# Kernel optimization log

Hardware: AMD Instinct MI355X
Metric: run time of the kernel (lower is better)

## Reference

```python
import jax, jax.numpy as jnp
import numpy as np

B, N, DIN, DMID, DOUT, E = 64, 5000, 64, 128, 32, 80000


def setup_inputs() -> dict:
    key = jax.random.key(0)
    ks = jax.random.split(key, 12)
    p = lambda k, shape: jax.random.normal(k, shape, jnp.float32) * 0.05
    return {
        "x": jax.random.normal(ks[0], (B, N, DIN), jnp.float32),
        "edge_index": jax.random.randint(ks[1], (2, E), 0, N),
        "prev_hidden_state": jax.random.normal(ks[2], (B, N, DMID), jnp.float32),
        # GCNConv weights/biases for gates z, r, h
        "Wg_z": p(ks[3], (DIN, DMID)), "bg_z": jnp.zeros((DMID,), jnp.float32),
        "Wg_r": p(ks[4], (DIN, DMID)), "bg_r": jnp.zeros((DMID,), jnp.float32),
        "Wg_h": p(ks[5], (DIN, DMID)), "bg_h": jnp.zeros((DMID,), jnp.float32),
        # gate Linear layers on concat([conv_out, H]) -> DMID
        "Wl_z": p(ks[6], (2 * DMID, DMID)), "bl_z": jnp.zeros((DMID,), jnp.float32),
        "Wl_r": p(ks[7], (2 * DMID, DMID)), "bl_r": jnp.zeros((DMID,), jnp.float32),
        "Wl_h": p(ks[8], (2 * DMID, DMID)), "bl_h": jnp.zeros((DMID,), jnp.float32),
        # final output Linear
        "W_out": p(ks[9], (DMID, DOUT)), "b_out": jnp.zeros((DOUT,), jnp.float32),
    }


def reference(x, edge_index, prev_hidden_state,
              Wg_z, bg_z, Wg_r, bg_r, Wg_h, bg_h,
              Wl_z, bl_z, Wl_r, bl_r, Wl_h, bl_h,
              W_out, b_out):
    # GCN symmetric normalization with self-loops (pyg gcn_norm, improved=False)
    row, col = edge_index[0], edge_index[1]
    loop = jnp.arange(N)
    src = jnp.concatenate([row, loop])          # [E+N]
    dst = jnp.concatenate([col, loop])          # [E+N]
    ew = jnp.ones((E + N,), x.dtype)
    deg = jnp.zeros((N,), x.dtype).at[dst].add(ew)
    dis = jnp.where(deg > 0, jax.lax.rsqrt(jnp.maximum(deg, 1e-12)), 0.0)
    norm = dis[src] * ew * dis[dst]             # [E+N]

    def gcn(w, b):
        xw = jnp.einsum('bnd,de->bne', x, w)            # [B,N,DMID]
        msg = xw[:, src, :] * norm[None, :, None]       # gather + weight
        out = jnp.zeros((B, N, w.shape[1]), x.dtype).at[:, dst, :].add(msg)
        return out + b

    H = prev_hidden_state
    Z = jax.nn.sigmoid(jnp.concatenate([gcn(Wg_z, bg_z), H], -1) @ Wl_z + bl_z)
    R = jax.nn.sigmoid(jnp.concatenate([gcn(Wg_r, bg_r), H], -1) @ Wl_r + bl_r)
    Ht = jnp.tanh(jnp.concatenate([gcn(Wg_h, bg_h), H * R], -1) @ Wl_h + bl_h)
    H_new = Z * H + (1.0 - Z) * Ht                      # [B,N,DMID]

    y = jnp.mean(H_new, axis=1)                         # MeanAggregation over nodes
    y = jax.nn.relu(y) @ W_out + b_out                  # [B,DOUT]
    return (y, H_new)
```

## Files before the change

### kernel.cpp

```cpp
#include <hip/hip_runtime.h>
#include <cmath>

namespace {

constexpr int B = 64, N = 5000, DIN = 64, DMID = 128, DOUT = 32, E = 80000;
constexpr int NT = (N + 63) / 64;

typedef unsigned short u16;
typedef __attribute__((ext_vector_type(8))) short short8;
typedef __attribute__((ext_vector_type(4))) float floatx4;

#define MFMA16(a, b, c) __builtin_amdgcn_mfma_f32_16x16x32_bf16((a), (b), (c), 0, 0, 0)

__device__ __forceinline__ u16 f2bf(float f) {
  union { float f; unsigned u; } v; v.f = f;
  unsigned r = v.u + 0x7FFFu + ((v.u >> 16) & 1u);
  return (u16)(r >> 16);
}
__device__ __forceinline__ float bf2f(u16 s) {
  union { unsigned u; float f; } v; v.u = ((unsigned)s) << 16;
  return v.f;
}
__device__ __forceinline__ float sigmoid_fast(float x) {
  return __builtin_amdgcn_rcpf(1.f + __expf(-x));
}
__device__ __forceinline__ float tanh_fast(float x) {
  return fmaf(2.f, __builtin_amdgcn_rcpf(1.f + __expf(-2.f * x)), -1.f);
}


__global__ void count_kernel(const int* __restrict__ ei, int* counts) {
  int e = blockIdx.x * 256 + threadIdx.x;
  if (e < E) atomicAdd(&counts[ei[E + e]], 1);
}

__global__ void scan_kernel(int* counts, int* rowptr, float* dis) {
  __shared__ int sdata[1024];
  const int tid = threadIdx.x;
  constexpr int CH = (N + 1023) / 1024;
  int local[CH], cnt[CH];
  int s = 0;
  for (int i = 0; i < CH; i++) {
    int idx = tid * CH + i;
    int c = (idx < N) ? counts[idx] : 0;
    cnt[i] = c;
    local[i] = s;
    s += c;
  }
  sdata[tid] = s;
  __syncthreads();
  for (int off = 1; off < 1024; off <<= 1) {
    int v = (tid >= off) ? sdata[tid - off] : 0;
    __syncthreads();
    sdata[tid] += v;
    __syncthreads();
  }
  int prev = (tid > 0) ? sdata[tid - 1] : 0;
  for (int i = 0; i < CH; i++) {
    int idx = tid * CH + i;
    if (idx < N) {
      rowptr[idx] = prev + local[i];
      dis[idx] = rsqrtf((float)(cnt[i] + 1));
      counts[idx] = 0;
    }
  }
  if (tid == 1023) rowptr[N] = sdata[1023];
}

__global__ void fill_kernel(const int* __restrict__ ei, const int* __restrict__ rowptr,
                            const float* __restrict__ dis, int* counts,
                            int* csr_src, float* csr_w) {
  int e = blockIdx.x * 256 + threadIdx.x;
  if (e >= E) return;
  int r = ei[e], c = ei[E + e];
  int pos = rowptr[c] + atomicAdd(&counts[c], 1);
  csr_src[pos] = r;
  csr_w[pos] = dis[r] * dis[c];
}


__global__ void pack_kernel(const float* Wgz, const float* Wgr, const float* Wgh,
                            const float* Wlz, const float* Wlr, const float* Wlh,
                            const float* bgz, const float* bgr, const float* bgh,
                            const float* blz, const float* blr, const float* blh,
                            u16* wcB, u16* whB, float* bcAll) {
  int t = blockIdx.x * 256 + threadIdx.x;
  const float* Wg[3] = {Wgz, Wgr, Wgh};
  const float* Wl[3] = {Wlz, Wlr, Wlh};
  const float* bg[3] = {bgz, bgr, bgh};
  const float* bl[3] = {blz, blr, blh};
  if (t < 48 * 64) {
    int chunk = t >> 6, lane = t & 63;
    int q = lane >> 4, lm = lane & 15;
    int g = chunk >> 4, rem = chunk & 15, kt = rem >> 3, nt = rem & 7;
    int n = nt * 16 + lm;
#pragma unroll
    for (int jj = 0; jj < 8; jj++) {
      int k = kt * 32 + q * 8 + jj;
      float acc = 0.f;
      for (int j = 0; j < DMID; j++)
        acc = fmaf(Wg[g][k * DMID + j], Wl[g][j * DMID + n], acc);
      wcB[(size_t)(chunk * 64 + lane) * 8 + jj] = f2bf(acc);
    }
  } else if (t < 48 * 64 + 96 * 64) {
    int t2 = t - 48 * 64;
    int chunk = t2 >> 6, lane = t2 & 63;
    int q = lane >> 4, lm = lane & 15;
    int g = chunk >> 5, rem = chunk & 31, kt = rem >> 3, nt = rem & 7;
    int n = nt * 16 + lm;
#pragma unroll
    for (int jj = 0; jj < 8; jj++) {
      int k = kt * 32 + q * 8 + jj;
      whB[(size_t)t2 * 8 + jj] = f2bf(Wl[g][(DMID + k) * DMID + n]);
    }
  } else {
    int t3 = t - 48 * 64 - 96 * 64;
    if (t3 < 384) {
      int g = t3 >> 7, n = t3 & 127;
      float acc = bl[g][n];
      for (int j = 0; j < DMID; j++)
        acc = fmaf(bg[g][j], Wl[g][j * DMID + n], acc);
      bcAll[t3] = acc;
    }
  }
}


__global__ __launch_bounds__(256) void agg_kernel(
    const float* __restrict__ x, const int* __restrict__ rowptr,
    const int* __restrict__ csr_src, const float* __restrict__ csr_w,
    const float* __restrict__ dis, u16* __restrict__ xs) {
  constexpr int G = B * N / 16;
  const int bid = blockIdx.x;
  const int nb = (bid & 7) * (G >> 3) + (bid >> 3);
  const int sub = threadIdx.x >> 4;
  const int l16 = threadIdx.x & 15;
  const int unit = nb * 16 + sub;
  const int b = unit / N;
  const int n = unit - b * N;
  const float* xb = x + (size_t)b * N * DIN;
  const float d = dis[n];
  float4 v = *(const float4*)(xb + (size_t)n * DIN + l16 * 4);
  const float sw = d * d;
  float ax = v.x * sw, ay = v.y * sw, az = v.z * sw, aw = v.w * sw;
  const int s1 = rowptr[n + 1];
  int p = rowptr[n];
  for (; p + 4 <= s1; p += 4) {
    int i0 = csr_src[p], i1 = csr_src[p + 1], i2 = csr_src[p + 2], i3 = csr_src[p + 3];
    float w0 = csr_w[p], w1 = csr_w[p + 1], w2 = csr_w[p + 2], w3 = csr_w[p + 3];
    float4 a0 = *(const float4*)(xb + (size_t)i0 * DIN + l16 * 4);
    float4 a1 = *(const float4*)(xb + (size_t)i1 * DIN + l16 * 4);
    float4 a2 = *(const float4*)(xb + (size_t)i2 * DIN + l16 * 4);
    float4 a3 = *(const float4*)(xb + (size_t)i3 * DIN + l16 * 4);
    ax = fmaf(a0.x, w0, ax); ay = fmaf(a0.y, w0, ay);
    az = fmaf(a0.z, w0, az); aw = fmaf(a0.w, w0, aw);
    ax = fmaf(a1.x, w1, ax); ay = fmaf(a1.y, w1, ay);
    az = fmaf(a1.z, w1, az); aw = fmaf(a1.w, w1, aw);
    ax = fmaf(a2.x, w2, ax); ay = fmaf(a2.y, w2, ay);
    az = fmaf(a2.z, w2, az); aw = fmaf(a2.w, w2, aw);
    ax = fmaf(a3.x, w3, ax); ay = fmaf(a3.y, w3, ay);
    az = fmaf(a3.z, w3, az); aw = fmaf(a3.w, w3, aw);
  }
  for (; p < s1; p++) {
    int i0 = csr_src[p];
    float w0 = csr_w[p];
    float4 a0 = *(const float4*)(xb + (size_t)i0 * DIN + l16 * 4);
    ax = fmaf(a0.x, w0, ax); ay = fmaf(a0.y, w0, ay);
    az = fmaf(a0.z, w0, az); aw = fmaf(a0.w, w0, aw);
  }
  uint2 o;
  o.x = (unsigned)f2bf(ax) | ((unsigned)f2bf(ay) << 16);
  o.y = (unsigned)f2bf(az) | ((unsigned)f2bf(aw) << 16);
  *(uint2*)(xs + (size_t)unit * DIN + l16 * 4) = o;
}


constexpr int SH = 136;

__global__ __launch_bounds__(256, 5) void fused_mfma(
    const u16* __restrict__ xs, const float* __restrict__ H,
    const u16* __restrict__ wcB, const u16* __restrict__ whB,
    const float* __restrict__ bcAll,
    float* __restrict__ hnew, float* __restrict__ partials) {
  __shared__ u16 H_s[64 * SH];

  const int tid = threadIdx.x;
  const int b = blockIdx.y;
  const int n0 = blockIdx.x * 64;
  const int lane = tid & 63, w = tid >> 6;
  const int q = lane >> 4, lm = lane & 15;
  const int w16 = w * 16;

#pragma unroll
  for (int j = 0; j < 8; j++) {
    int idx = j * 64 + lane;
    int rl = idx >> 5, seg = idx & 31;
    int row = w16 + rl;
    float4 v = make_float4(0.f, 0.f, 0.f, 0.f);
    if (n0 + row < N) v = *(const float4*)(H + ((size_t)b * N + n0 + row) * DMID + seg * 4);
    uint2 p;
    p.x = (unsigned)f2bf(v.x) | ((unsigned)f2bf(v.y) << 16);
    p.y = (unsigned)f2bf(v.z) | ((unsigned)f2bf(v.w) << 16);
    *(uint2*)&H_s[row * SH + seg * 4] = p;
  }

  const int an = n0 + w16 + lm;
  short8 ax[2];
  if (an < N) {
    const u16* xrow = xs + ((size_t)b * N + an) * DIN;
    ax[0] = *(const short8*)(xrow + q * 8);
    ax[1] = *(const short8*)(xrow + 32 + q * 8);
  } else {
    ax[0] = short8{0, 0, 0, 0, 0, 0, 0, 0};
    ax[1] = short8{0, 0, 0, 0, 0, 0, 0, 0};
  }

  short8 ah[4];
#pragma unroll
  for (int kt = 0; kt < 4; kt++)
    ah[kt] = *(const short8*)&H_s[(w16 + lm) * SH + kt * 32 + q * 8];

  floatx4 rpre[8];
#pragma unroll
  for (int nt = 0; nt < 8; nt++) {
    floatx4 a = {0.f, 0.f, 0.f, 0.f};
#pragma unroll
    for (int kt = 0; kt < 2; kt++)
      a = MFMA16(ax[kt], *(const short8*)(wcB + (size_t)((16 + kt * 8 + nt) * 64 + lane) * 8), a);
#pragma unroll
    for (int kt = 0; kt < 4; kt++)
      a = MFMA16(ah[kt], *(const short8*)(whB + (size_t)((32 + kt * 8 + nt) * 64 + lane) * 8), a);
    float bias = bcAll[128 + nt * 16 + lm];
#pragma unroll
    for (int r = 0; r < 4; r++) rpre[nt][r] = a[r] + bias;
  }

#pragma unroll
  for (int nt = 0; nt < 8; nt++)
#pragma unroll
    for (int r = 0; r < 4; r++) {
      int row = w16 + q * 4 + r, col = nt * 16 + lm;
      float h = bf2f(H_s[row * SH + col]);
      float rg = sigmoid_fast(rpre[nt][r]);
      H_s[row * SH + col] = f2bf(h * rg);
    }

  short8 ahr[4];
#pragma unroll
  for (int kt = 0; kt < 4; kt++)
    ahr[kt] = *(const short8*)&H_s[(w16 + lm) * SH + kt * 32 + q * 8];

#pragma unroll
  for (int nt = 0; nt < 8; nt++) {
    float hre[4];
#pragma unroll
    for (int r = 0; r < 4; r++) {
      int row = w16 + q * 4 + r;
      hre[r] = (n0 + row < N) ? H[((size_t)b * N + n0 + row) * DMID + nt * 16 + lm] : 0.f;
    }
    floatx4 za = {0.f, 0.f, 0.f, 0.f}, ha = {0.f, 0.f, 0.f, 0.f};
#pragma unroll
    for (int kt = 0; kt < 2; kt++) {
      za = MFMA16(ax[kt], *(const short8*)(wcB + (size_t)((0 + kt * 8 + nt) * 64 + lane) * 8), za);
      ha = MFMA16(ax[kt], *(const short8*)(wcB + (size_t)((32 + kt * 8 + nt) * 64 + lane) * 8), ha);
    }
#pragma unroll
    for (int kt = 0; kt < 4; kt++) {
      za = MFMA16(ah[kt], *(const short8*)(whB + (size_t)((0 + kt * 8 + nt) * 64 + lane) * 8), za);
      ha = MFMA16(ahr[kt], *(const short8*)(whB + (size_t)((64 + kt * 8 + nt) * 64 + lane) * 8), ha);
    }
    float zb = bcAll[nt * 16 + lm], hb = bcAll[256 + nt * 16 + lm];
    float colsum = 0.f;
#pragma unroll
    for (int r = 0; r < 4; r++) {
      int row = w16 + q * 4 + r;
      bool valid = (n0 + row) < N;
      float z = sigmoid_fast(za[r] + zb);
      float ht = tanh_fast(ha[r] + hb);
      float hn = fmaf(z, hre[r] - ht, ht);
      if (valid) {
        hnew[((size_t)b * N + n0 + row) * DMID + nt * 16 + lm] = hn;
        colsum += hn;
      }
    }
    colsum += __shfl_xor(colsum, 16);
    colsum += __shfl_xor(colsum, 32);
    if (lane < 16)
      partials[(((size_t)b * NT + blockIdx.x) * 4 + w) * DMID + nt * 16 + lane] = colsum;
  }
}


__global__ void out_kernel(const float* __restrict__ partials, const float* __restrict__ Wout,
                           const float* __restrict__ bout, float* __restrict__ y) {
  const int b = blockIdx.x;
  const int c = threadIdx.x;
  __shared__ float m[DMID];
  float acc = 0.f;
  for (int t = 0; t < NT * 4; t++)
    acc += partials[((size_t)b * NT * 4 + t) * DMID + c];
  m[c] = fmaxf(acc * (1.f / (float)N), 0.f);
  __syncthreads();
  if (c < DOUT) {
    float a2 = bout[c];
    for (int jj = 0; jj < DMID; jj++)
      a2 = fmaf(m[jj], Wout[jj * DOUT + c], a2);
    y[b * DOUT + c] = a2;
  }
}

}

extern "C" void kernel_launch(void* const* d_in, const int* in_sizes, int n_in,
                              void* d_out, int out_size, void* d_ws, size_t ws_size,
                              hipStream_t stream) {
  const float* x = (const float*)d_in[0];
  const int* ei = (const int*)d_in[1];
  const float* H = (const float*)d_in[2];
  const float* Wgz = (const float*)d_in[3];
  const float* bgz = (const float*)d_in[4];
  const float* Wgr = (const float*)d_in[5];
  const float* bgr = (const float*)d_in[6];
  const float* Wgh = (const float*)d_in[7];
  const float* bgh = (const float*)d_in[8];
  const float* Wlz = (const float*)d_in[9];
  const float* blz = (const float*)d_in[10];
  const float* Wlr = (const float*)d_in[11];
  const float* blr = (const float*)d_in[12];
  const float* Wlh = (const float*)d_in[13];
  const float* blh = (const float*)d_in[14];
  const float* Wout = (const float*)d_in[15];
  const float* bout = (const float*)d_in[16];

  float* y = (float*)d_out;
  float* hnew = (float*)d_out + (size_t)B * DOUT;

  char* p = (char*)d_ws;
  auto carve = [&](size_t bytes) {
    char* q = p;
    p += (bytes + 255) & ~size_t(255);
    return q;
  };
  int* counts = (int*)carve((size_t)N * 4);
  int* rowptr = (int*)carve((size_t)(N + 1) * 4);
  int* csr_src = (int*)carve((size_t)E * 4);
  float* csr_w = (float*)carve((size_t)E * 4);
  float* dis = (float*)carve((size_t)N * 4);
  u16* wcB = (u16*)carve((size_t)48 * 64 * 8 * 2);
  u16* whB = (u16*)carve((size_t)96 * 64 * 8 * 2);
  float* bcAll = (float*)carve((size_t)384 * 4);
  float* partials = (float*)carve((size_t)B * NT * 4 * DMID * 4);
  u16* xs = (u16*)carve((size_t)B * N * DIN * 2);

  hipMemsetAsync(counts, 0, (size_t)N * 4, stream);
  pack_kernel<<<38, 256, 0, stream>>>(Wgz, Wgr, Wgh, Wlz, Wlr, Wlh,
                                      bgz, bgr, bgh, blz, blr, blh,
                                      wcB, whB, bcAll);
  count_kernel<<<(E + 255) / 256, 256, 0, stream>>>(ei, counts);
  scan_kernel<<<1, 1024, 0, stream>>>(counts, rowptr, dis);
  fill_kernel<<<(E + 255) / 256, 256, 0, stream>>>(ei, rowptr, dis, counts, csr_src, csr_w);
  agg_kernel<<<B * N / 16, 256, 0, stream>>>(x, rowptr, csr_src, csr_w, dis, xs);
  fused_mfma<<<dim3(NT, B), 256, 0, stream>>>(xs, H, wcB, whB, bcAll, hnew, partials);
  out_kernel<<<B, DMID, 0, stream>>>(partials, Wout, bout, y);
}
```

Measured before the change: 736.4 us.

## Stash bf16 H in registers instead of re-reading fp32 H from global

The final gate blend now reuses the bf16 copy of H already held in shared memory, packed into registers during the reset-gate pass, instead of re-reading fp32 H from global memory. The z-gate MFMAs move before the candidate pass, so their preactivations stay in registers and the sigmoid for the reset gate is fused into its MFMA loop. The occupancy hint drops from 5 to 4 blocks per CU to leave room for the extra live registers. This removes one full fp32 read of H per element but uses H rounded to bf16 in the blend, which loses precision.

```diff
diff --git a/kernel.cpp b/kernel.cpp
--- a/kernel.cpp
+++ b/kernel.cpp
@@ -177,7 +177,7 @@
 
 constexpr int SH = 136;
 
-__global__ __launch_bounds__(256, 5) void fused_mfma(
+__global__ __launch_bounds__(256, 4) void fused_mfma(
     const u16* __restrict__ xs, const float* __restrict__ H,
     const u16* __restrict__ wcB, const u16* __restrict__ whB,
     const float* __restrict__ bcAll,
@@ -220,7 +220,7 @@
   for (int kt = 0; kt < 4; kt++)
     ah[kt] = *(const short8*)&H_s[(w16 + lm) * SH + kt * 32 + q * 8];
 
-  floatx4 rpre[8];
+  uint2 hstash[8];
 #pragma unroll
   for (int nt = 0; nt < 8; nt++) {
     floatx4 a = {0.f, 0.f, 0.f, 0.f};
@@ -231,19 +231,32 @@
     for (int kt = 0; kt < 4; kt++)
       a = MFMA16(ah[kt], *(const short8*)(whB + (size_t)((32 + kt * 8 + nt) * 64 + lane) * 8), a);
     float bias = bcAll[128 + nt * 16 + lm];
-#pragma unroll
-    for (int r = 0; r < 4; r++) rpre[nt][r] = a[r] + bias;
-  }
-
-#pragma unroll
-  for (int nt = 0; nt < 8; nt++)
+    unsigned hx = 0u, hy = 0u;
 #pragma unroll
     for (int r = 0; r < 4; r++) {
       int row = w16 + q * 4 + r, col = nt * 16 + lm;
-      float h = bf2f(H_s[row * SH + col]);
-      float rg = sigmoid_fast(rpre[nt][r]);
+      u16 hb = H_s[row * SH + col];
+      float h = bf2f(hb);
+      float rg = sigmoid_fast(a[r] + bias);
       H_s[row * SH + col] = f2bf(h * rg);
-    }
+      if (r < 2) hx |= ((unsigned)hb) << (16 * r);
+      else       hy |= ((unsigned)hb) << (16 * (r - 2));
+    }
+    hstash[nt] = make_uint2(hx, hy);
+  }
+
+  floatx4 zpre[8];
+#pragma unroll
+  for (int nt = 0; nt < 8; nt++) {
+    floatx4 a = {0.f, 0.f, 0.f, 0.f};
+#pragma unroll
+    for (int kt = 0; kt < 2; kt++)
+      a = MFMA16(ax[kt], *(const short8*)(wcB + (size_t)((0 + kt * 8 + nt) * 64 + lane) * 8), a);
+#pragma unroll
+    for (int kt = 0; kt < 4; kt++)
+      a = MFMA16(ah[kt], *(const short8*)(whB + (size_t)((0 + kt * 8 + nt) * 64 + lane) * 8), a);
+    zpre[nt] = a;
+  }
 
   short8 ahr[4];
 #pragma unroll
@@ -252,32 +265,24 @@
 
 #pragma unroll
   for (int nt = 0; nt < 8; nt++) {
-    float hre[4];
-#pragma unroll
-    for (int r = 0; r < 4; r++) {
-      int row = w16 + q * 4 + r;
-      hre[r] = (n0 + row < N) ? H[((size_t)b * N + n0 + row) * DMID + nt * 16 + lm] : 0.f;
-    }
-    floatx4 za = {0.f, 0.f, 0.f, 0.f}, ha = {0.f, 0.f, 0.f, 0.f};
-#pragma unroll
-    for (int kt = 0; kt < 2; kt++) {
-      za = MFMA16(ax[kt], *(const short8*)(wcB + (size_t)((0 + kt * 8 + nt) * 64 + lane) * 8), za);
+    floatx4 ha = {0.f, 0.f, 0.f, 0.f};
+#pragma unroll
+    for (int kt = 0; kt < 2; kt++)
       ha = MFMA16(ax[kt], *(const short8*)(wcB + (size_t)((32 + kt * 8 + nt) * 64 + lane) * 8), ha);
-    }
-#pragma unroll
-    for (int kt = 0; kt < 4; kt++) {
-      za = MFMA16(ah[kt], *(const short8*)(whB + (size_t)((0 + kt * 8 + nt) * 64 + lane) * 8), za);
+#pragma unroll
+    for (int kt = 0; kt < 4; kt++)
       ha = MFMA16(ahr[kt], *(const short8*)(whB + (size_t)((64 + kt * 8 + nt) * 64 + lane) * 8), ha);
-    }
-    float zb = bcAll[nt * 16 + lm], hb = bcAll[256 + nt * 16 + lm];
+    float zb = bcAll[nt * 16 + lm], hb_ = bcAll[256 + nt * 16 + lm];
     float colsum = 0.f;
 #pragma unroll
     for (int r = 0; r < 4; r++) {
       int row = w16 + q * 4 + r;
       bool valid = (n0 + row) < N;
-      float z = sigmoid_fast(za[r] + zb);
-      float ht = tanh_fast(ha[r] + hb);
-      float hn = fmaf(z, hre[r] - ht, ht);
+      unsigned word = (r < 2) ? hstash[nt].x : hstash[nt].y;
+      float h = bf2f((u16)(word >> (16 * (r & 1))));
+      float z = sigmoid_fast(zpre[nt][r] + zb);
+      float ht = tanh_fast(ha[r] + hb_);
+      float hn = fmaf(z, h - ht, ht);
       if (valid) {
         hnew[((size_t)b * N + n0 + row) * DMID + nt * 16 + lm] = hn;
         colsum += hn;
```

Measured after the change: 734.4 us. No clear change (-0.3%).
